# Performance work log

Measured on AMD Instinct MI355X. Metric: run time of the kernel, lower is better.

The kernel has to match this reference:

```python
import jax, jax.numpy as jnp
import numpy as np
import math

B, S, D, H = 1, 2048, 2048, 16
DH = D // H  # 128
HALF = DH // 2  # 64


def setup_inputs() -> dict:
    key = jax.random.key(0)
    ks = jax.random.split(key, 6)
    x = jax.random.normal(ks[0], (B, S, D), dtype=jnp.float32)
    # rotary frequencies: freqs_cis = exp(i * t * theta), theta_j = 10000^{-2j/DH}
    inv_freq = 1.0 / (10000.0 ** (np.arange(0, DH, 2, dtype=np.float32) / DH))  # [HALF]
    t = np.arange(S, dtype=np.float32)
    angles = np.outer(t, inv_freq)  # [S, HALF]
    freqs_cos = jnp.asarray(np.cos(angles), dtype=jnp.float32)
    freqs_sin = jnp.asarray(np.sin(angles), dtype=jnp.float32)
    # additive causal mask [1,1,S,S]
    mask = jnp.triu(jnp.full((S, S), -1e9, dtype=jnp.float32), k=1)[None, None]
    scale = 0.02
    wq = jax.random.normal(ks[1], (D, D), dtype=jnp.float32) * scale
    wk = jax.random.normal(ks[2], (D, D), dtype=jnp.float32) * scale
    wv = jax.random.normal(ks[3], (D, D), dtype=jnp.float32) * scale
    wo = jax.random.normal(ks[4], (D, D), dtype=jnp.float32) * scale
    return {"x": x, "freqs_cos": freqs_cos, "freqs_sin": freqs_sin, "mask": mask,
            "wq": wq, "wk": wk, "wv": wv, "wo": wo, "start_pos": 0}


def _apply_rope(t, cos, sin):
    # t: [B,S,H,DH]; cos/sin: [S,HALF] broadcast as [1,S,1,HALF]
    tr = t.reshape(*t.shape[:-1], HALF, 2)
    even, odd = tr[..., 0], tr[..., 1]
    c = cos[None, :, None, :]
    s = sin[None, :, None, :]
    out_even = even * c - odd * s
    out_odd = even * s + odd * c
    return jnp.stack([out_even, out_odd], axis=-1).reshape(t.shape)


def reference(x, freqs_cos, freqs_sin, mask, wq, wk, wv, wo, start_pos):
    bsz, seqlen, _ = x.shape
    q = (x @ wq.T).reshape(bsz, seqlen, H, DH)
    k = (x @ wk.T).reshape(bsz, seqlen, H, DH)
    v = (x @ wv.T).reshape(bsz, seqlen, H, DH)
    q = _apply_rope(q, freqs_cos, freqs_sin)
    k = _apply_rope(k, freqs_cos, freqs_sin)
    q = q.transpose(0, 2, 1, 3)  # [B,H,S,DH]
    k = k.transpose(0, 2, 1, 3)
    v = v.transpose(0, 2, 1, 3)
    scores = jnp.einsum('bhqd,bhkd->bhqk', q, k) / math.sqrt(DH) + mask
    probs = jax.nn.softmax(scores, axis=-1)
    out = jnp.einsum('bhqk,bhkd->bhqd', probs, v)  # [B,H,S,DH]
    # faithful to original: transpose(2,3) then view(bsz, seqlen, dim)
    out = out.transpose(0, 1, 3, 2).reshape(bsz, seqlen, D)
    return out @ wo.T
```

## Files before the change

kernel.cpp:

```cpp
#include <hip/hip_runtime.h>

typedef unsigned short u16;
typedef unsigned int   u32;
typedef short  short8   __attribute__((ext_vector_type(8)));
typedef float  floatx4  __attribute__((ext_vector_type(4)));
typedef u16    ushortx2 __attribute__((ext_vector_type(2)));
typedef u16    ushortx4 __attribute__((ext_vector_type(4)));

__device__ __forceinline__ float bf2f(u16 u) {
  union { u32 i; float f; } v; v.i = ((u32)u) << 16; return v.f;
}
__device__ __forceinline__ u16 f2bf(float x) {
  union { float f; u32 i; } v; v.f = x;
  u32 r = v.i + 0x7FFFu + ((v.i >> 16) & 1u);
  return (u16)(r >> 16);
}

#if __has_builtin(__builtin_amdgcn_exp2f)
#define EXP2F(x) __builtin_amdgcn_exp2f(x)
#else
#define EXP2F(x) __exp2f(x)
#endif

#define GLOAD_LDS16(gptr, lptr)                                                   \
  __builtin_amdgcn_global_load_lds(                                               \
      (const __attribute__((address_space(1))) void*)(gptr),                      \
      (__attribute__((address_space(3))) void*)(lptr), 16, 0, 0)

__global__ __launch_bounds__(256) void cvt_all(
    const floatx4* __restrict__ x,  const floatx4* __restrict__ wq,
    const floatx4* __restrict__ wk, const floatx4* __restrict__ wv,
    const floatx4* __restrict__ wo,
    ushortx4* __restrict__ xb, ushortx4* __restrict__ wqkv,
    ushortx4* __restrict__ wob) {
  int i = blockIdx.x * 256 + threadIdx.x;
  const floatx4* in; ushortx4* out;
  switch (blockIdx.y) {
    case 0:  in = x;  out = xb; break;
    case 1:  in = wq; out = wqkv; break;
    case 2:  in = wk; out = wqkv + (size_t)1048576; break;
    case 3:  in = wv; out = wqkv + (size_t)2097152; break;
    default: in = wo; out = wob; break;
  }
  floatx4 v = in[i];
  ushortx4 o;
  o.x = f2bf(v.x); o.y = f2bf(v.y); o.z = f2bf(v.z); o.w = f2bf(v.w);
  out[i] = o;
}

__global__ __launch_bounds__(256) void gemm_bt(
    const u16* __restrict__ A, const u16* __restrict__ B, void* __restrict__ Cv,
    int M, int N, int K, int lda, int ldb, int ldc,
    long batchA, long batchB, long batchC, int outBF16) {
  const int m0 = blockIdx.y << 7;
  const int n0 = blockIdx.x << 7;

  A += (long)blockIdx.z * batchA;
  B += (long)blockIdx.z * batchB;
  const long cbase = (long)blockIdx.z * batchC;

  __shared__ __align__(16) u16 As[128][64];
  __shared__ __align__(16) u16 Bs[128][64];

  const int t = threadIdx.x;
  const int lane = t & 63;
  const int wave = t >> 6;
  const int wm = (wave >> 1) << 6;
  const int wn = (wave & 1) << 6;
  const int quad = lane >> 4;
  const int mrow = lane & 15;
  const int sw8 = mrow & 7;

  floatx4 acc[4][4] = {};

  const int srow = lane >> 3;
  const int gseg = (((lane & 7) ^ srow) << 3);
  const u16* gA = A + (long)(m0 + (wave << 5) + srow) * lda + gseg;
  const u16* gB = B + (long)(n0 + (wave << 5) + srow) * ldb + gseg;

  for (int k0 = 0; k0 < K; k0 += 64) {
    __syncthreads();
#pragma unroll
    for (int ii = 0; ii < 4; ii++) {
      GLOAD_LDS16(gA + k0 + (size_t)(ii << 3) * lda, &As[(wave << 5) + (ii << 3)][0]);
      GLOAD_LDS16(gB + k0 + (size_t)(ii << 3) * ldb, &Bs[(wave << 5) + (ii << 3)][0]);
    }
    __syncthreads();

#pragma unroll
    for (int kh = 0; kh < 2; kh++) {
      const int sidx = ((kh << 2) | quad) ^ sw8;
      short8 af[4], bfr[4];
#pragma unroll
      for (int i = 0; i < 4; i++)
        af[i] = *(const short8*)&As[wm + (i << 4) + mrow][sidx << 3];
#pragma unroll
      for (int j = 0; j < 4; j++)
        bfr[j] = *(const short8*)&Bs[wn + (j << 4) + mrow][sidx << 3];
#pragma unroll
      for (int i = 0; i < 4; i++)
#pragma unroll
        for (int j = 0; j < 4; j++)
          acc[i][j] = __builtin_amdgcn_mfma_f32_16x16x32_bf16(af[i], bfr[j], acc[i][j], 0, 0, 0);
    }
  }

#pragma unroll
  for (int i = 0; i < 4; i++) {
    int row0 = m0 + wm + (i << 4) + (quad << 2);
#pragma unroll
    for (int j = 0; j < 4; j++) {
      int col = n0 + wn + (j << 4) + mrow;
#pragma unroll
      for (int r = 0; r < 4; r++) {
        long idx = cbase + (long)(row0 + r) * ldc + col;
        float val = acc[i][j][r];
        if (outBF16) ((u16*)Cv)[idx] = f2bf(val);
        else         ((float*)Cv)[idx] = val;
      }
    }
  }
}

__global__ __launch_bounds__(256) void transpose_v(const u16* __restrict__ src,
                                                   u16* __restrict__ dst) {
  __shared__ u16 tile[64][68];
  const int d0 = blockIdx.x << 6;
  const int s0 = blockIdx.y << 6;
  const int tx = (threadIdx.x & 15) << 2;
  const int ty = threadIdx.x >> 4;
#pragma unroll
  for (int rr = 0; rr < 64; rr += 16) {
    ushortx4 v = *(const ushortx4*)(src + (size_t)(s0 + ty + rr) * 6144 + d0 + tx);
    *(ushortx4*)&tile[ty + rr][tx] = v;
  }
  __syncthreads();
#pragma unroll
  for (int rr = 0; rr < 64; rr += 16) {
    int r = ty + rr;
    ushortx4 o;
    o.x = tile[tx + 0][r]; o.y = tile[tx + 1][r];
    o.z = tile[tx + 2][r]; o.w = tile[tx + 3][r];
    *(ushortx4*)(dst + (size_t)(d0 + r) * 2048 + s0 + tx) = o;
  }
}

__global__ __launch_bounds__(256) void rope_qk(u16* __restrict__ qkv,
                                               const float* __restrict__ cs,
                                               const float* __restrict__ sn) {
  int idx = blockIdx.x * 256 + threadIdx.x;
  int p = idx & 63;
  int h = (idx >> 6) & 15;
  int s = idx >> 10;
  float c  = cs[(s << 6) | p];
  float si = sn[(s << 6) | p];
  float scale = blockIdx.y ? 1.0f : 0.12751743f;
  size_t off = (size_t)s * 6144 + (blockIdx.y ? 2048 : 0) + (h << 7) + (p << 1);
  ushortx2 eo = *(ushortx2*)(qkv + off);
  float e = bf2f(eo.x), o = bf2f(eo.y);
  ushortx2 r;
  r.x = f2bf((e * c - o * si) * scale);
  r.y = f2bf((e * si + o * c) * scale);
  *(ushortx2*)(qkv + off) = r;
}

__global__ __launch_bounds__(256, 2) void flash_attn(
    const u16* __restrict__ QKVp, const u16* __restrict__ VTp,
    u16* __restrict__ ATp) {
  const int r0id = (int)blockIdx.x + ((int)blockIdx.y << 5);
  const int h    = r0id & 15;
  const int qsub = 31 - (r0id >> 4);
  const int q0 = qsub << 6;
  const int ktmax = qsub >> 1;

  __shared__ __align__(16) u16 Ks[128][128];
  __shared__ __align__(16) u16 Vs[128][128];
  __shared__ __align__(16) u16 Ps[64][128];

  const int t = threadIdx.x;
  const int lane = t & 63;
  const int wave = t >> 6;
  const int quad = lane >> 4;
  const int mrow = lane & 15;
  const int sw   = mrow & 7;
  const int wmS = (wave & 1) << 5;
  const int wnS = (wave >> 1) << 6;
  const int wmV = (wave >> 1) << 6;
  const int wnP = (wave & 1) << 5;

  const int r4  = lane >> 4;
  const int seg = lane & 15;
  const int c0 = ((seg ^ r4) << 3);
  const int c4 = ((seg ^ (r4 + 4)) << 3);

  const u16* qbase = QKVp + (size_t)q0 * 6144 + (h << 7);
  const u16* kbase = QKVp + 2048 + (h << 7);
  const u16* vbase = VTp + (size_t)(h << 7) * 2048;

  short8 aq[2][4];
#pragma unroll
  for (int i = 0; i < 2; i++)
#pragma unroll
    for (int kk = 0; kk < 4; kk++)
      aq[i][kk] = *(const short8*)(qbase + (size_t)(wmS + (i << 4) + mrow) * 6144 +
                                   (kk << 5) + (quad << 3));

  const short8 ones = {0x3F80, 0x3F80, 0x3F80, 0x3F80,
                       0x3F80, 0x3F80, 0x3F80, 0x3F80};

  floatx4 Oa[4][2] = {};
  floatx4 Oa1[2] = {};

  const float C2 = 23.083120654223414f;

  for (int kt = 0; kt <= ktmax; kt++) {
    __syncthreads();
    {
      int rr0 = wave << 5;
#pragma unroll
      for (int ii = 0; ii < 8; ii++) {
        int rr = rr0 + (ii << 2);
        GLOAD_LDS16(kbase + (size_t)((kt << 7) + rr + r4) * 6144 + ((ii & 1) ? c4 : c0),
                    &Ks[rr][0]);
        GLOAD_LDS16(vbase + (size_t)(rr + r4) * 2048 + (kt << 7) + ((ii & 1) ? c4 : c0),
                    &Vs[rr][0]);
      }
    }
    __syncthreads();

    floatx4 sa[2][4] = {};
#pragma unroll
    for (int kk = 0; kk < 4; kk++) {
      short8 bk[4];
#pragma unroll
      for (int j = 0; j < 4; j++)
        bk[j] = *(const short8*)&Ks[wnS + (j << 4) + mrow][(((kk << 2) | quad) ^ sw) << 3];
#pragma unroll
      for (int i = 0; i < 2; i++)
#pragma unroll
        for (int j = 0; j < 4; j++)
          sa[i][j] = __builtin_amdgcn_mfma_f32_16x16x32_bf16(aq[i][kk], bk[j], sa[i][j], 0, 0, 0);
    }
    if (kt == ktmax) {
#pragma unroll
      for (int i = 0; i < 2; i++)
#pragma unroll
        for (int j = 0; j < 4; j++)
#pragma unroll
          for (int r = 0; r < 4; r++) {
            int ql = q0 + wmS + (i << 4) + (quad << 2) + r;
            int sl = (kt << 7) + wnS + (j << 4) + mrow;
            if (sl > ql) sa[i][j][r] = -1e30f;
          }
    }
#pragma unroll
    for (int i = 0; i < 2; i++)
#pragma unroll
      for (int j = 0; j < 4; j++)
#pragma unroll
        for (int r = 0; r < 4; r++) {
          int row = wmS + (i << 4) + (quad << 2) + r;
          int col = wnS + (j << 4) + mrow;
          Ps[row][((((col >> 3) ^ (row & 7)) << 3) | (col & 7))] =
              f2bf(EXP2F(sa[i][j][r] - C2));
        }
    __syncthreads();

#pragma unroll
    for (int kk = 0; kk < 4; kk++) {
      short8 av[4], bp[2];
#pragma unroll
      for (int i = 0; i < 4; i++)
        av[i] = *(const short8*)&Vs[wmV + (i << 4) + mrow][(((kk << 2) | quad) ^ sw) << 3];
#pragma unroll
      for (int j = 0; j < 2; j++)
        bp[j] = *(const short8*)&Ps[wnP + (j << 4) + mrow][(((kk << 2) | quad) ^ sw) << 3];
#pragma unroll
      for (int i = 0; i < 4; i++)
#pragma unroll
        for (int j = 0; j < 2; j++)
          Oa[i][j] = __builtin_amdgcn_mfma_f32_16x16x32_bf16(av[i], bp[j], Oa[i][j], 0, 0, 0);
#pragma unroll
      for (int j = 0; j < 2; j++)
        Oa1[j] = __builtin_amdgcn_mfma_f32_16x16x32_bf16(ones, bp[j], Oa1[j], 0, 0, 0);
    }
  }

  float linv[2];
#pragma unroll
  for (int j = 0; j < 2; j++) linv[j] = 1.f / Oa1[j][0];
#pragma unroll
  for (int i = 0; i < 4; i++) {
    int drow = (h << 7) + wmV + (i << 4) + (quad << 2);
#pragma unroll
    for (int j = 0; j < 2; j++) {
      int col = q0 + wnP + (j << 4) + mrow;
#pragma unroll
      for (int r = 0; r < 4; r++)
        ATp[(size_t)(drow + r) * 2048 + col] = f2bf(Oa[i][j][r] * linv[j]);
    }
  }
}

__global__ __launch_bounds__(256) void reduce2(const floatx4* __restrict__ a,
                                               const floatx4* __restrict__ b,
                                               floatx4* __restrict__ o) {
  int i = blockIdx.x * 256 + threadIdx.x;
  o[i] = a[i] + b[i];
}

extern "C" void kernel_launch(void* const* d_in, const int* in_sizes, int n_in,
                              void* d_out, int out_size, void* d_ws, size_t ws_size,
                              hipStream_t stream) {
  const float* x  = (const float*)d_in[0];
  const float* fc = (const float*)d_in[1];
  const float* fs = (const float*)d_in[2];
  const float* wq = (const float*)d_in[4];
  const float* wk = (const float*)d_in[5];
  const float* wv = (const float*)d_in[6];
  const float* wo = (const float*)d_in[7];
  float* out = (float*)d_out;

  char* ws = (char*)d_ws;
  const size_t MB = 1024 * 1024;
  u16*   XB   = (u16*)(ws + 0 * MB);
  u16*   WQKV = (u16*)(ws + 8 * MB);
  u16*   WOb  = (u16*)(ws + 32 * MB);
  u16*   QKV  = (u16*)(ws + 40 * MB);
  u16*   VT   = (u16*)(ws + 64 * MB);
  u16*   AT   = (u16*)(ws + 72 * MB);
  float* PART = (float*)(ws + 80 * MB);

  int use_split = (ws_size >= 113 * MB);

  dim3 blk(256);
  cvt_all<<<dim3(4096, 5), blk, 0, stream>>>(
      (const floatx4*)x, (const floatx4*)wq, (const floatx4*)wk,
      (const floatx4*)wv, (const floatx4*)wo,
      (ushortx4*)XB, (ushortx4*)WQKV, (ushortx4*)WOb);

  gemm_bt<<<dim3(48, 16, 1), blk, 0, stream>>>(XB, WQKV, QKV, 2048, 6144, 2048,
                                               2048, 2048, 6144, 0, 0, 0, 1);

  transpose_v<<<dim3(32, 32), blk, 0, stream>>>(QKV + 4096, VT);
  rope_qk<<<dim3(8192, 2), blk, 0, stream>>>(QKV, fc, fs);

  flash_attn<<<dim3(32, 16), blk, 0, stream>>>(QKV, VT, AT);

  if (use_split) {
    gemm_bt<<<dim3(16, 16, 2), blk, 0, stream>>>(AT, WOb, PART, 2048, 2048, 1024,
                                                 2048, 2048, 2048,
                                                 1024, 1024, (long)2048 * 2048, 0);
    reduce2<<<4096, blk, 0, stream>>>((const floatx4*)PART,
                                      (const floatx4*)(PART + (size_t)2048 * 2048),
                                      (floatx4*)out);
  } else {
    gemm_bt<<<dim3(16, 16, 1), blk, 0, stream>>>(AT, WOb, out, 2048, 2048, 2048,
                                                 2048, 2048, 2048, 0, 0, 0, 0);
  }
}
```

Baseline: 303.8 us.

## Use 256x256 double-buffered 8-wave GEMM for fused QKV projection

Adds a new GEMM kernel that computes 256x256 output tiles with 512 threads. It double-buffers LDS using direct global-to-LDS loads with XOR swizzling, interleaves quarter-tile MFMA groups with the next tile's loads, and remaps block indices across XCDs. It replaces the 128x128 GEMM for the QKV projection. The goal is more data reuse per LDS load and better overlap of memory with compute. In exchange it uses 128KB of LDS, a grid of only 192 blocks, and a hand-tuned waitcnt/barrier schedule that is delicate to get right.

```diff
diff --git a/kernel.cpp b/kernel.cpp
--- a/kernel.cpp
+++ b/kernel.cpp
@@ -26,6 +26,10 @@
   __builtin_amdgcn_global_load_lds(                                               \
       (const __attribute__((address_space(1))) void*)(gptr),                      \
       (__attribute__((address_space(3))) void*)(lptr), 16, 0, 0)
+
+#define WAITV(n) asm volatile("s_waitcnt vmcnt(" #n ")" ::: "memory")
+#define WAITL    asm volatile("s_waitcnt lgkmcnt(0)" ::: "memory")
+#define BAR      __builtin_amdgcn_s_barrier()
 
 __global__ __launch_bounds__(256) void cvt_all(
     const floatx4* __restrict__ x,  const floatx4* __restrict__ wq,
@@ -46,6 +50,144 @@
   ushortx4 o;
   o.x = f2bf(v.x); o.y = f2bf(v.y); o.z = f2bf(v.z); o.w = f2bf(v.w);
   out[i] = o;
+}
+
+__global__ __launch_bounds__(512, 2) void gemm256_bt(
+    const u16* __restrict__ A, const u16* __restrict__ B, u16* __restrict__ C,
+    int N, int K, int lda, int ldb, int ldc) {
+  const int cpx = gridDim.x >> 3;
+  const int wg = ((int)blockIdx.x & 7) * cpx + ((int)blockIdx.x >> 3);
+  const int ntn = N >> 8;
+  const int m0 = (wg / ntn) << 8;
+  const int n0 = (wg % ntn) << 8;
+
+  __shared__ __align__(16) u16 As[2][256][64];
+  __shared__ __align__(16) u16 Bs[2][256][64];
+
+  const int t = threadIdx.x;
+  const int lane = t & 63;
+  const int wave = t >> 6;
+  const int wr = wave >> 2;
+  const int wc = wave & 3;
+  const int quad = lane >> 4;
+  const int mrow = lane & 15;
+  const int sw = mrow & 7;
+
+  const int srow = lane >> 3;
+  const int gso  = ((lane & 7) ^ srow) << 3;
+
+  const u16* gA = A + (size_t)(m0 + (wave << 3) + srow) * lda + gso;
+  const u16* gB = B + (size_t)(n0 + (wave << 3) + srow) * ldb + gso;
+
+  floatx4 acc[8][4] = {};
+  short8 afr[4][2], bfr[4][2];
+
+  const int NT = K >> 6;
+
+#define ST_A(nb, h, kt)                                                        \
+  do {                                                                         \
+    GLOAD_LDS16(gA + (size_t)((h) * 128) * lda + ((kt) << 6),                  \
+                &As[nb][(h) * 128 + (wave << 3)][0]);                          \
+    GLOAD_LDS16(gA + (size_t)((h) * 128 + 64) * lda + ((kt) << 6),             \
+                &As[nb][(h) * 128 + 64 + (wave << 3)][0]);                     \
+  } while (0)
+#define ST_B(nb, h, kt)                                                        \
+  do {                                                                         \
+    GLOAD_LDS16(gB + (size_t)((h) * 128) * ldb + ((kt) << 6),                  \
+                &Bs[nb][(h) * 128 + (wave << 3)][0]);                          \
+    GLOAD_LDS16(gB + (size_t)((h) * 128 + 64) * ldb + ((kt) << 6),             \
+                &Bs[nb][(h) * 128 + 64 + (wave << 3)][0]);                     \
+  } while (0)
+
+#define LDA4(bf, base_row)                                                     \
+  do {                                                                         \
+    _Pragma("unroll") for (int i_ = 0; i_ < 4; i_++)                           \
+      _Pragma("unroll") for (int kk_ = 0; kk_ < 2; kk_++)                      \
+        afr[i_][kk_] = *(const short8*)&As[bf][(base_row) + (i_ << 4) + mrow]  \
+                            [(((kk_ << 2) | quad) ^ sw) << 3];                 \
+  } while (0)
+#define LDB2(bf, jlo, base_row)                                                \
+  do {                                                                         \
+    _Pragma("unroll") for (int j_ = 0; j_ < 2; j_++)                           \
+      _Pragma("unroll") for (int kk_ = 0; kk_ < 2; kk_++)                      \
+        bfr[(jlo) + j_][kk_] =                                                 \
+            *(const short8*)&Bs[bf][(base_row) + (j_ << 4) + mrow]             \
+                [(((kk_ << 2) | quad) ^ sw) << 3];                             \
+  } while (0)
+#define MMQ(ilo, jlo)                                                          \
+  do {                                                                         \
+    __builtin_amdgcn_s_setprio(1);                                             \
+    _Pragma("unroll") for (int kk_ = 0; kk_ < 2; kk_++)                        \
+      _Pragma("unroll") for (int i_ = 0; i_ < 4; i_++)                         \
+        _Pragma("unroll") for (int j_ = 0; j_ < 2; j_++)                       \
+          acc[(ilo) + i_][(jlo) + j_] =                                        \
+              __builtin_amdgcn_mfma_f32_16x16x32_bf16(                         \
+                  afr[i_][kk_], bfr[(jlo) + j_][kk_],                          \
+                  acc[(ilo) + i_][(jlo) + j_], 0, 0, 0);                       \
+    __builtin_amdgcn_s_setprio(0);                                             \
+  } while (0)
+
+  ST_A(0, 0, 0); ST_B(0, 0, 0); ST_B(0, 1, 0); ST_A(0, 1, 0);
+  WAITV(4);
+  BAR;
+
+  for (int kt = 0; kt < NT - 1; kt++) {
+    const int bf = kt & 1, nb = bf ^ 1;
+    LDA4(bf, (wr << 6));
+    LDB2(bf, 0, (wc << 5));
+    ST_A(nb, 0, kt + 1);
+    WAITV(4);
+    BAR;
+    MMQ(0, 0);
+    LDB2(bf, 2, 128 + (wc << 5));
+    ST_B(nb, 0, kt + 1);
+    WAITV(4);
+    BAR;
+    MMQ(0, 2);
+    LDA4(bf, 128 + (wr << 6));
+    ST_B(nb, 1, kt + 1);
+    BAR;
+    MMQ(4, 2);
+    ST_A(nb, 1, kt + 1);
+    WAITL;
+    WAITV(4);
+    BAR;
+    MMQ(4, 0);
+  }
+  {
+    const int bf = (NT - 1) & 1;
+    LDA4(bf, (wr << 6));
+    LDB2(bf, 0, (wc << 5));
+    WAITV(2);
+    BAR;
+    MMQ(0, 0);
+    LDB2(bf, 2, 128 + (wc << 5));
+    WAITV(0);
+    BAR;
+    MMQ(0, 2);
+    LDA4(bf, 128 + (wr << 6));
+    WAITL;
+    BAR;
+    MMQ(4, 2);
+    MMQ(4, 0);
+  }
+
+#pragma unroll
+  for (int i = 0; i < 8; i++) {
+    int row0 = m0 + ((i >= 4) ? 128 : 0) + (wr << 6) + ((i & 3) << 4) + (quad << 2);
+#pragma unroll
+    for (int j = 0; j < 4; j++) {
+      int col = n0 + ((j >= 2) ? 128 : 0) + (wc << 5) + ((j & 1) << 4) + mrow;
+#pragma unroll
+      for (int r = 0; r < 4; r++)
+        C[(size_t)(row0 + r) * ldc + col] = f2bf(acc[i][j][r]);
+    }
+  }
+#undef ST_A
+#undef ST_B
+#undef LDA4
+#undef LDB2
+#undef MMQ
 }
 
 __global__ __launch_bounds__(256) void gemm_bt(
@@ -339,8 +481,8 @@
       (const floatx4*)wv, (const floatx4*)wo,
       (ushortx4*)XB, (ushortx4*)WQKV, (ushortx4*)WOb);
 
-  gemm_bt<<<dim3(48, 16, 1), blk, 0, stream>>>(XB, WQKV, QKV, 2048, 6144, 2048,
-                                               2048, 2048, 6144, 0, 0, 0, 1);
+  gemm256_bt<<<dim3(192), dim3(512), 0, stream>>>(XB, WQKV, QKV,
+                                                  6144, 2048, 2048, 2048, 6144);
 
   transpose_v<<<dim3(32, 32), blk, 0, stream>>>(QKV + 4096, VT);
   rope_qk<<<dim3(8192, 2), blk, 0, stream>>>(QKV, fc, fs);
```

Measured after the change: 289.1 us. -4.8%, faster.
